# Performance work log

Hardware: AMD Instinct MI355X
Metric: run time of the kernel (lower is better)

The kernel has to match this reference:

```python
import jax, jax.numpy as jnp
import numpy as np

NUM_ELECTIONS = 4096  # number of segments (elections)
N_VOTERS = 1048576
NUM_CANDIDATES = 32
EMB = 128


def setup_inputs() -> dict:
    key = jax.random.key(0)
    ks = jax.random.split(key, 9)
    s = lambda k, sh: jax.random.normal(k, sh, dtype=jnp.float32) * 0.05
    x = jax.random.normal(ks[0], (N_VOTERS, NUM_CANDIDATES), dtype=jnp.float32)
    index = jnp.sort(jax.random.randint(ks[1], (N_VOTERS,), 0, NUM_ELECTIONS)).astype(jnp.int64)
    return {
        "x": x,
        "index": index,
        "lW1": s(ks[2], (NUM_CANDIDATES, EMB)), "lb1": jnp.zeros((EMB,), jnp.float32),
        "lW2": s(ks[3], (EMB, EMB)),            "lb2": jnp.zeros((EMB,), jnp.float32),
        "lW3": s(ks[4], (EMB, EMB)),            "lb3": jnp.zeros((EMB,), jnp.float32),
        "gW1": s(ks[5], (EMB, EMB)),            "gb1": jnp.zeros((EMB,), jnp.float32),
        "gW2": s(ks[6], (EMB, EMB)),            "gb2": jnp.zeros((EMB,), jnp.float32),
        "gW3": s(ks[7], (EMB, NUM_CANDIDATES)), "gb3": jnp.zeros((NUM_CANDIDATES,), jnp.float32),
    }


def reference(x, index, lW1, lb1, lW2, lb2, lW3, lb3, gW1, gb1, gW2, gb2, gW3, gb3):
    # local_nn per voter row: MLP [C, E, E, E], ReLU on hidden layers, plain last
    h = jax.nn.relu(x @ lW1 + lb1)
    h = jax.nn.relu(h @ lW2 + lb2)
    h = h @ lW3 + lb3                      # [N, E]
    # scatter-sum aggregation by election id (DeepSetsAggregation sum reduce)
    agg = jax.ops.segment_sum(h, index, num_segments=NUM_ELECTIONS)  # [S, E]
    # global_nn: MLP [E, E, E, C]
    g = jax.nn.relu(agg @ gW1 + gb1)
    g = jax.nn.relu(g @ gW2 + gb2)
    scores = g @ gW3 + gb3                 # [S, C]
    return jax.nn.log_softmax(scores, axis=-1)
```

## Files before the change

### kernel.cpp

```cpp
#include <hip/hip_runtime.h>
#include <hip/hip_bf16.h>
#include <math.h>

#define N_VOTERS 1048576
#define NUM_CAND 32
#define EMB 128
#define NUM_ELEC 4096

typedef unsigned short u16;
typedef unsigned int u32;
typedef __attribute__((ext_vector_type(8))) short bf16x8;
typedef __attribute__((ext_vector_type(4))) short short4v;
typedef __attribute__((ext_vector_type(4))) float f32x4;

__device__ __forceinline__ u16 f2bf(float f) {
    union { float f; u32 u; } v; v.f = f;
    u32 r = v.u + 0x7FFFu + ((v.u >> 16) & 1u);
    return (u16)(r >> 16);
}
__device__ __forceinline__ u32 pkbf(float f0, float f1) {
    u32 u0 = __float_as_uint(f0) + 0x8000u;
    u32 u1 = __float_as_uint(f1) + 0x8000u;
    return __builtin_amdgcn_perm(u1, u0, 0x07060302u);
}

__global__ void prep_weights(const float* __restrict__ lW1, const float* __restrict__ lW2,
                             const float* __restrict__ lW3,
                             u16* __restrict__ w1t, u16* __restrict__ w2t, u16* __restrict__ w3t) {
    int tid = blockIdx.x * blockDim.x + threadIdx.x;
    if (tid < 4096) {
        int n = tid >> 5, k = tid & 31;
        w1t[tid] = f2bf(lW1[k * EMB + n]);
    }
    {
        int n = tid >> 7, k = tid & 127;
        w2t[tid] = f2bf(lW2[k * EMB + n]);
        w3t[tid] = f2bf(lW3[k * EMB + n]);
    }
}

__global__ __launch_bounds__(256, 4) void local_fused(
    const float* __restrict__ x, const int* __restrict__ idx,
    const float* __restrict__ lb1, const float* __restrict__ lb2, const float* __restrict__ lb3,
    const u16* __restrict__ w1t, const u16* __restrict__ w2t, const u16* __restrict__ w3t,
    float* __restrict__ agg)
{
    constexpr int XSTR = 36;
    constexpr int ASTR = 136;
    __shared__ __align__(16) u16 smem[64 * XSTR + 2 * 64 * ASTR];
    __shared__ int segs[64];
    u16* bufX = smem;
    u16* act1 = smem + 64 * XSTR;
    u16* act2 = act1 + 64 * ASTR;

    const int tid = threadIdx.x;
    const int v0 = blockIdx.x * 64;
    const int lane = tid & 63;
    const int wv = tid >> 6;
    const int qd = lane >> 4;
    const int l15 = lane & 15;
    const int mrow0 = wv * 32 + l15;

    {
        const float4* xin = (const float4*)(x + (size_t)v0 * NUM_CAND);
        #pragma unroll
        for (int i = 0; i < 2; ++i) {
            int F = i * 256 + tid;
            float4 v = xin[F];
            int row = F >> 3, c4 = (F & 7) * 4;
            uint2 pv; pv.x = pkbf(v.x, v.y); pv.y = pkbf(v.z, v.w);
            *(uint2*)(bufX + row * XSTR + c4) = pv;
        }
        if (tid < 64) segs[tid] = idx[v0 + tid];
    }

    bf16x8 wa0 = *(const bf16x8*)(w1t + mrow0 * 32 + qd * 8);
    bf16x8 wa1 = *(const bf16x8*)(w1t + (mrow0 + 16) * 32 + qd * 8);
    f32x4 bA1 = *(const f32x4*)(lb1 + wv * 32 + qd * 4);
    f32x4 bB1 = *(const f32x4*)(lb1 + wv * 32 + 16 + qd * 4);
    __syncthreads();

    #pragma unroll
    for (int nt = 0; nt < 4; ++nt) {
        int vr = nt * 16 + l15;
        union { bf16x8 v; short4v h[2]; } b;
        b.h[0] = *(const short4v*)(bufX + vr * XSTR + qd * 8);
        b.h[1] = *(const short4v*)(bufX + vr * XSTR + qd * 8 + 4);
        f32x4 z = {0.f, 0.f, 0.f, 0.f};
        f32x4 a0 = __builtin_amdgcn_mfma_f32_16x16x32_bf16(wa0, b.v, z, 0, 0, 0);
        f32x4 a1 = __builtin_amdgcn_mfma_f32_16x16x32_bf16(wa1, b.v, z, 0, 0, 0);
        uint2 s0; s0.x = pkbf(fmaxf(a0[0] + bA1[0], 0.f), fmaxf(a0[1] + bA1[1], 0.f));
        s0.y = pkbf(fmaxf(a0[2] + bA1[2], 0.f), fmaxf(a0[3] + bA1[3], 0.f));
        *(uint2*)(act1 + vr * ASTR + wv * 32 + qd * 4) = s0;
        uint2 s1; s1.x = pkbf(fmaxf(a1[0] + bB1[0], 0.f), fmaxf(a1[1] + bB1[1], 0.f));
        s1.y = pkbf(fmaxf(a1[2] + bB1[2], 0.f), fmaxf(a1[3] + bB1[3], 0.f));
        *(uint2*)(act1 + vr * ASTR + wv * 32 + 16 + qd * 4) = s1;
    }

    bf16x8 w2a[2][4];
    #pragma unroll
    for (int t = 0; t < 2; ++t)
        #pragma unroll
        for (int kk = 0; kk < 4; ++kk)
            w2a[t][kk] = *(const bf16x8*)(w2t + (mrow0 + t * 16) * 128 + kk * 32 + qd * 8);
    f32x4 bA2 = *(const f32x4*)(lb2 + wv * 32 + qd * 4);
    f32x4 bB2 = *(const f32x4*)(lb2 + wv * 32 + 16 + qd * 4);
    __syncthreads();

    #pragma unroll
    for (int nt = 0; nt < 4; ++nt) {
        int vr = nt * 16 + l15;
        f32x4 a0 = {0.f, 0.f, 0.f, 0.f}, a1 = {0.f, 0.f, 0.f, 0.f};
        #pragma unroll
        for (int kk = 0; kk < 4; ++kk) {
            bf16x8 b = *(const bf16x8*)(act1 + vr * ASTR + kk * 32 + qd * 8);
            a0 = __builtin_amdgcn_mfma_f32_16x16x32_bf16(w2a[0][kk], b, a0, 0, 0, 0);
            a1 = __builtin_amdgcn_mfma_f32_16x16x32_bf16(w2a[1][kk], b, a1, 0, 0, 0);
        }
        uint2 s0; s0.x = pkbf(fmaxf(a0[0] + bA2[0], 0.f), fmaxf(a0[1] + bA2[1], 0.f));
        s0.y = pkbf(fmaxf(a0[2] + bA2[2], 0.f), fmaxf(a0[3] + bA2[3], 0.f));
        *(uint2*)(act2 + vr * ASTR + wv * 32 + qd * 4) = s0;
        uint2 s1; s1.x = pkbf(fmaxf(a1[0] + bB2[0], 0.f), fmaxf(a1[1] + bB2[1], 0.f));
        s1.y = pkbf(fmaxf(a1[2] + bB2[2], 0.f), fmaxf(a1[3] + bB2[3], 0.f));
        *(uint2*)(act2 + vr * ASTR + wv * 32 + 16 + qd * 4) = s1;
    }

    bf16x8 w3a[2][4];
    #pragma unroll
    for (int t = 0; t < 2; ++t)
        #pragma unroll
        for (int kk = 0; kk < 4; ++kk)
            w3a[t][kk] = *(const bf16x8*)(w3t + (mrow0 + t * 16) * 128 + kk * 32 + qd * 8);
    f32x4 bA3 = *(const f32x4*)(lb3 + wv * 32 + qd * 4);
    f32x4 bB3 = *(const f32x4*)(lb3 + wv * 32 + 16 + qd * 4);
    __syncthreads();

    float fs0[4] = {0.f, 0.f, 0.f, 0.f}, fs1[4] = {0.f, 0.f, 0.f, 0.f};
    int cnt = 0;
    int cur = segs[0];
    float* const aggb = agg + (size_t)wv * 32 + qd * 4;

    auto flush = [&]() {
        float t[8];
        #pragma unroll
        for (int r = 0; r < 4; ++r) { t[r] = fs0[r]; t[4 + r] = fs1[r]; }
        #pragma unroll
        for (int d = 1; d < 16; d <<= 1)
            #pragma unroll
            for (int r = 0; r < 8; ++r) t[r] += __shfl_xor(t[r], d, 16);
        if (l15 == 0) {
            float c = (float)(cnt * 16);
            float* p = aggb + (size_t)cur * EMB;
            #pragma unroll
            for (int r = 0; r < 4; ++r) atomicAdd(p + r,      fmaf(bA3[r], c, t[r]));
            #pragma unroll
            for (int r = 0; r < 4; ++r) atomicAdd(p + 16 + r, fmaf(bB3[r], c, t[4 + r]));
        }
        #pragma unroll
        for (int r = 0; r < 4; ++r) { fs0[r] = 0.f; fs1[r] = 0.f; }
        cnt = 0;
    };

    #pragma unroll
    for (int nt = 0; nt < 4; ++nt) {
        int vr = nt * 16 + l15;
        f32x4 a0 = {0.f, 0.f, 0.f, 0.f}, a1 = {0.f, 0.f, 0.f, 0.f};
        #pragma unroll
        for (int kk = 0; kk < 4; ++kk) {
            bf16x8 b = *(const bf16x8*)(act2 + vr * ASTR + kk * 32 + qd * 8);
            a0 = __builtin_amdgcn_mfma_f32_16x16x32_bf16(w3a[0][kk], b, a0, 0, 0, 0);
            a1 = __builtin_amdgcn_mfma_f32_16x16x32_bf16(w3a[1][kk], b, a1, 0, 0, 0);
        }
        int sg = segs[nt * 16 + l15];
        int first = __builtin_amdgcn_readfirstlane(sg);
        unsigned long long bal = __ballot(sg == first);
        if (bal == ~0ull) {
            if (first != cur) {
                if (cnt > 0) flush();
                cur = first;
            }
            #pragma unroll
            for (int r = 0; r < 4; ++r) { fs0[r] += a0[r]; fs1[r] += a1[r]; }
            ++cnt;
        } else {
            if (cnt > 0) flush();
            float v0a[4], v1a[4];
            #pragma unroll
            for (int r = 0; r < 4; ++r) { v0a[r] = a0[r] + bA3[r]; v1a[r] = a1[r] + bB3[r]; }
            #pragma unroll
            for (int d = 1; d < 16; d <<= 1) {
                int so = __shfl_up(sg, d, 16);
                bool ok = (l15 >= d) && (so == sg);
                #pragma unroll
                for (int r = 0; r < 4; ++r) {
                    float o0 = __shfl_up(v0a[r], d, 16); if (ok) v0a[r] += o0;
                    float o1 = __shfl_up(v1a[r], d, 16); if (ok) v1a[r] += o1;
                }
            }
            int sgn = __shfl_down(sg, 1, 16);
            bool isend = (l15 == 15) || (sgn != sg);
            if (isend) {
                float* p = aggb + (size_t)sg * EMB;
                #pragma unroll
                for (int r = 0; r < 4; ++r) atomicAdd(p + r,      v0a[r]);
                #pragma unroll
                for (int r = 0; r < 4; ++r) atomicAdd(p + 16 + r, v1a[r]);
            }
            cur = __shfl(sg, 15, 16);
        }
    }
    if (cnt > 0) flush();
}

__global__ __launch_bounds__(256) void global_mlp(
    const float* __restrict__ agg,
    const float* __restrict__ gW1, const float* __restrict__ gb1,
    const float* __restrict__ gW2, const float* __restrict__ gb2,
    const float* __restrict__ gW3, const float* __restrict__ gb3,
    float* __restrict__ out)
{
    __shared__ float actA[8 * 128];
    __shared__ float actB[8 * 128];
    __shared__ float sc[8 * 32];
    const int tid = threadIdx.x;
    const int s0 = blockIdx.x * 8;

    #pragma unroll
    for (int i = 0; i < 4; ++i) {
        int f = i * 256 + tid;
        actA[f] = agg[(size_t)s0 * 128 + f];
    }
    __syncthreads();

    const int j = tid & 127, g = tid >> 7;
    {
        float acc[4];
        #pragma unroll
        for (int si = 0; si < 4; ++si) acc[si] = gb1[j];
        #pragma unroll 8
        for (int k = 0; k < 128; ++k) {
            float w = gW1[k * 128 + j];
            #pragma unroll
            for (int si = 0; si < 4; ++si) acc[si] += actA[(g * 4 + si) * 128 + k] * w;
        }
        #pragma unroll
        for (int si = 0; si < 4; ++si) actB[(g * 4 + si) * 128 + j] = fmaxf(acc[si], 0.f);
    }
    __syncthreads();
    {
        float acc[4];
        #pragma unroll
        for (int si = 0; si < 4; ++si) acc[si] = gb2[j];
        #pragma unroll 8
        for (int k = 0; k < 128; ++k) {
            float w = gW2[k * 128 + j];
            #pragma unroll
            for (int si = 0; si < 4; ++si) acc[si] += actB[(g * 4 + si) * 128 + k] * w;
        }
        #pragma unroll
        for (int si = 0; si < 4; ++si) actA[(g * 4 + si) * 128 + j] = fmaxf(acc[si], 0.f);
    }
    __syncthreads();
    {
        int c = tid & 31, sg = tid >> 5;
        float a3 = gb3[c];
        #pragma unroll 8
        for (int k = 0; k < 128; ++k) a3 += actA[sg * 128 + k] * gW3[k * 32 + c];
        sc[sg * 32 + c] = a3;
    }
    __syncthreads();
    {
        int c = tid & 31, sg = tid >> 5;
        float v = sc[sg * 32 + c];
        float m = v;
        #pragma unroll
        for (int off = 16; off >= 1; off >>= 1) m = fmaxf(m, __shfl_xor(m, off, 32));
        float e = expf(v - m);
        float sum = e;
        #pragma unroll
        for (int off = 16; off >= 1; off >>= 1) sum += __shfl_xor(sum, off, 32);
        out[(size_t)(s0 + sg) * 32 + c] = (v - m) - logf(sum);
    }
}

extern "C" void kernel_launch(void* const* d_in, const int* in_sizes, int n_in,
                              void* d_out, int out_size, void* d_ws, size_t ws_size,
                              hipStream_t stream) {
    const float* x   = (const float*)d_in[0];
    const int*   idx = (const int*)d_in[1];
    const float* lW1 = (const float*)d_in[2];
    const float* lb1 = (const float*)d_in[3];
    const float* lW2 = (const float*)d_in[4];
    const float* lb2 = (const float*)d_in[5];
    const float* lW3 = (const float*)d_in[6];
    const float* lb3 = (const float*)d_in[7];
    const float* gW1 = (const float*)d_in[8];
    const float* gb1 = (const float*)d_in[9];
    const float* gW2 = (const float*)d_in[10];
    const float* gb2 = (const float*)d_in[11];
    const float* gW3 = (const float*)d_in[12];
    const float* gb3 = (const float*)d_in[13];
    float* out = (float*)d_out;

    float* agg = (float*)d_ws;
    u16* w1t = (u16*)((char*)d_ws + (size_t)NUM_ELEC * EMB * 4);
    u16* w2t = w1t + 128 * 32;
    u16* w3t = w2t + 128 * 128;

    hipMemsetAsync(d_ws, 0, (size_t)NUM_ELEC * EMB * sizeof(float), stream);
    prep_weights<<<64, 256, 0, stream>>>(lW1, lW2, lW3, w1t, w2t, w3t);
    local_fused<<<N_VOTERS / 64, 256, 0, stream>>>(x, idx, lb1, lb2, lb3, w1t, w2t, w3t, agg);
    global_mlp<<<NUM_ELEC / 8, 256, 0, stream>>>(agg, gW1, gb1, gW2, gb2, gW3, gb3, out);
}
```

Baseline: 352.2 us.

## Keep local MLP activations in registers with per-wave full-width tiles and LDS-resident weights

Restructures the local MLP kernel so each wave computes all 128 output features for its own 64 voters. Inter-layer activations are passed through cross-lane shuffles instead of LDS round trips, and all three weight matrices sit in shared memory for 512-thread blocks. The last-layer bias is folded into the global MLP through per-segment voter counts, and the next x tile is prefetched into registers. It removes the LDS activation staging and block-wide barriers between layers, at the cost of many shuffles, high register pressure from the 8x4 accumulators, and reloading the weights into LDS for every block.

```diff
diff --git a/kernel.cpp b/kernel.cpp
--- a/kernel.cpp
+++ b/kernel.cpp
@@ -10,8 +10,9 @@
 typedef unsigned short u16;
 typedef unsigned int u32;
 typedef __attribute__((ext_vector_type(8))) short bf16x8;
-typedef __attribute__((ext_vector_type(4))) short short4v;
 typedef __attribute__((ext_vector_type(4))) float f32x4;
+
+union U4 { u32 u[4]; bf16x8 v; };
 
 __device__ __forceinline__ u16 f2bf(float f) {
     union { float f; u32 u; } v; v.f = f;
@@ -39,181 +40,246 @@
     }
 }
 
-__global__ __launch_bounds__(256, 4) void local_fused(
+__global__ __launch_bounds__(512, 4) void local_fused(
     const float* __restrict__ x, const int* __restrict__ idx,
-    const float* __restrict__ lb1, const float* __restrict__ lb2, const float* __restrict__ lb3,
+    const float* __restrict__ lb1, const float* __restrict__ lb2,
     const u16* __restrict__ w1t, const u16* __restrict__ w2t, const u16* __restrict__ w3t,
-    float* __restrict__ agg)
+    float* __restrict__ agg, float* __restrict__ cntf)
 {
-    constexpr int XSTR = 36;
-    constexpr int ASTR = 136;
-    __shared__ __align__(16) u16 smem[64 * XSTR + 2 * 64 * ASTR];
-    __shared__ int segs[64];
-    u16* bufX = smem;
-    u16* act1 = smem + 64 * XSTR;
-    u16* act2 = act1 + 64 * ASTR;
+    __shared__ __align__(16) u16 w1s[128 * 32];
+    __shared__ __align__(16) u16 w2s[128 * 128];
+    __shared__ __align__(16) u16 w3s[128 * 128];
+    __shared__ __align__(16) float lb1s[128], lb2s[128];
 
     const int tid = threadIdx.x;
-    const int v0 = blockIdx.x * 64;
+
+    {
+        const uint4* s2 = (const uint4*)w2t; uint4* d2 = (uint4*)w2s;
+        const uint4* s3 = (const uint4*)w3t; uint4* d3 = (uint4*)w3s;
+        #pragma unroll
+        for (int i = 0; i < 4; ++i) {
+            d2[tid + i * 512] = s2[tid + i * 512];
+            d3[tid + i * 512] = s3[tid + i * 512];
+        }
+        ((uint4*)w1s)[tid] = ((const uint4*)w1t)[tid];
+        if (tid < 128) { lb1s[tid] = lb1[tid]; lb2s[tid] = lb2[tid]; }
+    }
+    __syncthreads();
+
     const int lane = tid & 63;
     const int wv = tid >> 6;
     const int qd = lane >> 4;
     const int l15 = lane & 15;
-    const int mrow0 = wv * 32 + l15;
-
-    {
-        const float4* xin = (const float4*)(x + (size_t)v0 * NUM_CAND);
-        #pragma unroll
-        for (int i = 0; i < 2; ++i) {
-            int F = i * 256 + tid;
-            float4 v = xin[F];
-            int row = F >> 3, c4 = (F & 7) * 4;
-            uint2 pv; pv.x = pkbf(v.x, v.y); pv.y = pkbf(v.z, v.w);
-            *(uint2*)(bufX + row * XSTR + c4) = pv;
-        }
-        if (tid < 64) segs[tid] = idx[v0 + tid];
-    }
-
-    bf16x8 wa0 = *(const bf16x8*)(w1t + mrow0 * 32 + qd * 8);
-    bf16x8 wa1 = *(const bf16x8*)(w1t + (mrow0 + 16) * 32 + qd * 8);
-    f32x4 bA1 = *(const f32x4*)(lb1 + wv * 32 + qd * 4);
-    f32x4 bB1 = *(const f32x4*)(lb1 + wv * 32 + 16 + qd * 4);
-    __syncthreads();
-
+    const int vb = blockIdx.x * 512 + wv * 64;
+
+    const int s0l = ((qd & 1) << 5) + l15;
+    const int s1l = s0l + 16;
+    const bool hi = (qd >> 1) != 0;
+
+    float fs[8][4];
     #pragma unroll
+    for (int m = 0; m < 8; ++m)
+        #pragma unroll
+        for (int r = 0; r < 4; ++r) fs[m][r] = 0.f;
+    float cntv = 0.f;
+    int cur = idx[vb];
+
+    const float* xr0 = x + (size_t)(vb + l15) * NUM_CAND + qd * 8;
+    float4 xa = *(const float4*)xr0;
+    float4 xb = *(const float4*)(xr0 + 4);
+
+    #pragma unroll 1
     for (int nt = 0; nt < 4; ++nt) {
-        int vr = nt * 16 + l15;
-        union { bf16x8 v; short4v h[2]; } b;
-        b.h[0] = *(const short4v*)(bufX + vr * XSTR + qd * 8);
-        b.h[1] = *(const short4v*)(bufX + vr * XSTR + qd * 8 + 4);
-        f32x4 z = {0.f, 0.f, 0.f, 0.f};
-        f32x4 a0 = __builtin_amdgcn_mfma_f32_16x16x32_bf16(wa0, b.v, z, 0, 0, 0);
-        f32x4 a1 = __builtin_amdgcn_mfma_f32_16x16x32_bf16(wa1, b.v, z, 0, 0, 0);
-        uint2 s0; s0.x = pkbf(fmaxf(a0[0] + bA1[0], 0.f), fmaxf(a0[1] + bA1[1], 0.f));
-        s0.y = pkbf(fmaxf(a0[2] + bA1[2], 0.f), fmaxf(a0[3] + bA1[3], 0.f));
-        *(uint2*)(act1 + vr * ASTR + wv * 32 + qd * 4) = s0;
-        uint2 s1; s1.x = pkbf(fmaxf(a1[0] + bB1[0], 0.f), fmaxf(a1[1] + bB1[1], 0.f));
-        s1.y = pkbf(fmaxf(a1[2] + bB1[2], 0.f), fmaxf(a1[3] + bB1[3], 0.f));
-        *(uint2*)(act1 + vr * ASTR + wv * 32 + 16 + qd * 4) = s1;
-    }
-
-    bf16x8 w2a[2][4];
-    #pragma unroll
-    for (int t = 0; t < 2; ++t)
-        #pragma unroll
-        for (int kk = 0; kk < 4; ++kk)
-            w2a[t][kk] = *(const bf16x8*)(w2t + (mrow0 + t * 16) * 128 + kk * 32 + qd * 8);
-    f32x4 bA2 = *(const f32x4*)(lb2 + wv * 32 + qd * 4);
-    f32x4 bB2 = *(const f32x4*)(lb2 + wv * 32 + 16 + qd * 4);
-    __syncthreads();
-
-    #pragma unroll
-    for (int nt = 0; nt < 4; ++nt) {
-        int vr = nt * 16 + l15;
-        f32x4 a0 = {0.f, 0.f, 0.f, 0.f}, a1 = {0.f, 0.f, 0.f, 0.f};
+        int sg = idx[vb + nt * 16 + l15];
+        int ntn = (nt < 3) ? nt + 1 : 3;
+        const float* xrn = x + (size_t)(vb + ntn * 16 + l15) * NUM_CAND + qd * 8;
+        float4 xa_n = *(const float4*)xrn;
+        float4 xb_n = *(const float4*)(xrn + 4);
+
+        U4 B1; B1.u[0] = pkbf(xa.x, xa.y); B1.u[1] = pkbf(xa.z, xa.w);
+        B1.u[2] = pkbf(xb.x, xb.y); B1.u[3] = pkbf(xb.z, xb.w);
+
+        f32x4 D[8];
+        #pragma unroll
+        for (int mt = 0; mt < 8; ++mt) {
+            bf16x8 A = *(const bf16x8*)(w1s + (mt * 16 + l15) * 32 + qd * 8);
+            f32x4 z = {0.f, 0.f, 0.f, 0.f};
+            D[mt] = __builtin_amdgcn_mfma_f32_16x16x32_bf16(A, B1.v, z, 0, 0, 0);
+        }
+        u32 P[8][2];
+        #pragma unroll
+        for (int mt = 0; mt < 8; ++mt) {
+            f32x4 b = *(const f32x4*)(lb1s + mt * 16 + qd * 4);
+            float v0 = fmaxf(D[mt][0] + b[0], 0.f), v1 = fmaxf(D[mt][1] + b[1], 0.f);
+            float v2 = fmaxf(D[mt][2] + b[2], 0.f), v3 = fmaxf(D[mt][3] + b[3], 0.f);
+            P[mt][0] = pkbf(v0, v1); P[mt][1] = pkbf(v2, v3);
+        }
+        U4 Bf[4];
         #pragma unroll
         for (int kk = 0; kk < 4; ++kk) {
-            bf16x8 b = *(const bf16x8*)(act1 + vr * ASTR + kk * 32 + qd * 8);
-            a0 = __builtin_amdgcn_mfma_f32_16x16x32_bf16(w2a[0][kk], b, a0, 0, 0, 0);
-            a1 = __builtin_amdgcn_mfma_f32_16x16x32_bf16(w2a[1][kk], b, a1, 0, 0, 0);
-        }
-        uint2 s0; s0.x = pkbf(fmaxf(a0[0] + bA2[0], 0.f), fmaxf(a0[1] + bA2[1], 0.f));
-        s0.y = pkbf(fmaxf(a0[2] + bA2[2], 0.f), fmaxf(a0[3] + bA2[3], 0.f));
-        *(uint2*)(act2 + vr * ASTR + wv * 32 + qd * 4) = s0;
-        uint2 s1; s1.x = pkbf(fmaxf(a1[0] + bB2[0], 0.f), fmaxf(a1[1] + bB2[1], 0.f));
-        s1.y = pkbf(fmaxf(a1[2] + bB2[2], 0.f), fmaxf(a1[3] + bB2[3], 0.f));
-        *(uint2*)(act2 + vr * ASTR + wv * 32 + 16 + qd * 4) = s1;
-    }
-
-    bf16x8 w3a[2][4];
-    #pragma unroll
-    for (int t = 0; t < 2; ++t)
-        #pragma unroll
-        for (int kk = 0; kk < 4; ++kk)
-            w3a[t][kk] = *(const bf16x8*)(w3t + (mrow0 + t * 16) * 128 + kk * 32 + qd * 8);
-    f32x4 bA3 = *(const f32x4*)(lb3 + wv * 32 + qd * 4);
-    f32x4 bB3 = *(const f32x4*)(lb3 + wv * 32 + 16 + qd * 4);
-    __syncthreads();
-
-    float fs0[4] = {0.f, 0.f, 0.f, 0.f}, fs1[4] = {0.f, 0.f, 0.f, 0.f};
-    int cnt = 0;
-    int cur = segs[0];
-    float* const aggb = agg + (size_t)wv * 32 + qd * 4;
-
-    auto flush = [&]() {
-        float t[8];
-        #pragma unroll
-        for (int r = 0; r < 4; ++r) { t[r] = fs0[r]; t[4 + r] = fs1[r]; }
-        #pragma unroll
-        for (int d = 1; d < 16; d <<= 1)
-            #pragma unroll
-            for (int r = 0; r < 8; ++r) t[r] += __shfl_xor(t[r], d, 16);
-        if (l15 == 0) {
-            float c = (float)(cnt * 16);
-            float* p = aggb + (size_t)cur * EMB;
-            #pragma unroll
-            for (int r = 0; r < 4; ++r) atomicAdd(p + r,      fmaf(bA3[r], c, t[r]));
-            #pragma unroll
-            for (int r = 0; r < 4; ++r) atomicAdd(p + 16 + r, fmaf(bB3[r], c, t[4 + r]));
-        }
-        #pragma unroll
-        for (int r = 0; r < 4; ++r) { fs0[r] = 0.f; fs1[r] = 0.f; }
-        cnt = 0;
-    };
-
-    #pragma unroll
-    for (int nt = 0; nt < 4; ++nt) {
-        int vr = nt * 16 + l15;
-        f32x4 a0 = {0.f, 0.f, 0.f, 0.f}, a1 = {0.f, 0.f, 0.f, 0.f};
+            u32 e0 = __shfl(P[2 * kk][0], s0l, 64), o0 = __shfl(P[2 * kk + 1][0], s0l, 64);
+            u32 e1 = __shfl(P[2 * kk][1], s0l, 64), o1 = __shfl(P[2 * kk + 1][1], s0l, 64);
+            u32 e2 = __shfl(P[2 * kk][0], s1l, 64), o2 = __shfl(P[2 * kk + 1][0], s1l, 64);
+            u32 e3 = __shfl(P[2 * kk][1], s1l, 64), o3 = __shfl(P[2 * kk + 1][1], s1l, 64);
+            Bf[kk].u[0] = hi ? o0 : e0; Bf[kk].u[1] = hi ? o1 : e1;
+            Bf[kk].u[2] = hi ? o2 : e2; Bf[kk].u[3] = hi ? o3 : e3;
+        }
+        #pragma unroll
+        for (int mt = 0; mt < 8; ++mt) {
+            f32x4 a = {0.f, 0.f, 0.f, 0.f};
+            #pragma unroll
+            for (int kk = 0; kk < 4; ++kk) {
+                bf16x8 A = *(const bf16x8*)(w2s + (mt * 16 + l15) * 128 + kk * 32 + qd * 8);
+                a = __builtin_amdgcn_mfma_f32_16x16x32_bf16(A, Bf[kk].v, a, 0, 0, 0);
+            }
+            D[mt] = a;
+        }
+        #pragma unroll
+        for (int mt = 0; mt < 8; ++mt) {
+            f32x4 b = *(const f32x4*)(lb2s + mt * 16 + qd * 4);
+            float v0 = fmaxf(D[mt][0] + b[0], 0.f), v1 = fmaxf(D[mt][1] + b[1], 0.f);
+            float v2 = fmaxf(D[mt][2] + b[2], 0.f), v3 = fmaxf(D[mt][3] + b[3], 0.f);
+            P[mt][0] = pkbf(v0, v1); P[mt][1] = pkbf(v2, v3);
+        }
         #pragma unroll
         for (int kk = 0; kk < 4; ++kk) {
-            bf16x8 b = *(const bf16x8*)(act2 + vr * ASTR + kk * 32 + qd * 8);
-            a0 = __builtin_amdgcn_mfma_f32_16x16x32_bf16(w3a[0][kk], b, a0, 0, 0, 0);
-            a1 = __builtin_amdgcn_mfma_f32_16x16x32_bf16(w3a[1][kk], b, a1, 0, 0, 0);
-        }
-        int sg = segs[nt * 16 + l15];
+            u32 e0 = __shfl(P[2 * kk][0], s0l, 64), o0 = __shfl(P[2 * kk + 1][0], s0l, 64);
+            u32 e1 = __shfl(P[2 * kk][1], s0l, 64), o1 = __shfl(P[2 * kk + 1][1], s0l, 64);
+            u32 e2 = __shfl(P[2 * kk][0], s1l, 64), o2 = __shfl(P[2 * kk + 1][0], s1l, 64);
+            u32 e3 = __shfl(P[2 * kk][1], s1l, 64), o3 = __shfl(P[2 * kk + 1][1], s1l, 64);
+            Bf[kk].u[0] = hi ? o0 : e0; Bf[kk].u[1] = hi ? o1 : e1;
+            Bf[kk].u[2] = hi ? o2 : e2; Bf[kk].u[3] = hi ? o3 : e3;
+        }
+        #pragma unroll
+        for (int mt = 0; mt < 8; ++mt) {
+            f32x4 a = {0.f, 0.f, 0.f, 0.f};
+            #pragma unroll
+            for (int kk = 0; kk < 4; ++kk) {
+                bf16x8 A = *(const bf16x8*)(w3s + (mt * 16 + l15) * 128 + kk * 32 + qd * 8);
+                a = __builtin_amdgcn_mfma_f32_16x16x32_bf16(A, Bf[kk].v, a, 0, 0, 0);
+            }
+            D[mt] = a;
+        }
+
+        xa = xa_n; xb = xb_n;
+
         int first = __builtin_amdgcn_readfirstlane(sg);
         unsigned long long bal = __ballot(sg == first);
         if (bal == ~0ull) {
             if (first != cur) {
-                if (cnt > 0) flush();
+                if (cntv > 0.f) {
+                    float t[8][4];
+                    #pragma unroll
+                    for (int m = 0; m < 8; ++m)
+                        #pragma unroll
+                        for (int r = 0; r < 4; ++r) t[m][r] = fs[m][r];
+                    #pragma unroll
+                    for (int d = 1; d < 16; d <<= 1)
+                        #pragma unroll
+                        for (int m = 0; m < 8; ++m)
+                            #pragma unroll
+                            for (int r = 0; r < 4; ++r) t[m][r] += __shfl_xor(t[m][r], d, 16);
+                    if (l15 == 0) {
+                        float* p = agg + (size_t)cur * EMB + qd * 4;
+                        #pragma unroll
+                        for (int m = 0; m < 8; ++m)
+                            #pragma unroll
+                            for (int r = 0; r < 4; ++r) atomicAdd(p + m * 16 + r, t[m][r]);
+                        if (qd == 0) atomicAdd(cntf + cur, cntv);
+                    }
+                    #pragma unroll
+                    for (int m = 0; m < 8; ++m)
+                        #pragma unroll
+                        for (int r = 0; r < 4; ++r) fs[m][r] = 0.f;
+                    cntv = 0.f;
+                }
                 cur = first;
             }
             #pragma unroll
-            for (int r = 0; r < 4; ++r) { fs0[r] += a0[r]; fs1[r] += a1[r]; }
-            ++cnt;
+            for (int m = 0; m < 8; ++m)
+                #pragma unroll
+                for (int r = 0; r < 4; ++r) fs[m][r] += D[m][r];
+            cntv += 16.f;
         } else {
-            if (cnt > 0) flush();
-            float v0a[4], v1a[4];
-            #pragma unroll
-            for (int r = 0; r < 4; ++r) { v0a[r] = a0[r] + bA3[r]; v1a[r] = a1[r] + bB3[r]; }
+            if (cntv > 0.f) {
+                float t[8][4];
+                #pragma unroll
+                for (int m = 0; m < 8; ++m)
+                    #pragma unroll
+                    for (int r = 0; r < 4; ++r) t[m][r] = fs[m][r];
+                #pragma unroll
+                for (int d = 1; d < 16; d <<= 1)
+                    #pragma unroll
+                    for (int m = 0; m < 8; ++m)
+                        #pragma unroll
+                        for (int r = 0; r < 4; ++r) t[m][r] += __shfl_xor(t[m][r], d, 16);
+                if (l15 == 0) {
+                    float* p = agg + (size_t)cur * EMB + qd * 4;
+                    #pragma unroll
+                    for (int m = 0; m < 8; ++m)
+                        #pragma unroll
+                        for (int r = 0; r < 4; ++r) atomicAdd(p + m * 16 + r, t[m][r]);
+                    if (qd == 0) atomicAdd(cntf + cur, cntv);
+                }
+                #pragma unroll
+                for (int m = 0; m < 8; ++m)
+                    #pragma unroll
+                    for (int r = 0; r < 4; ++r) fs[m][r] = 0.f;
+                cntv = 0.f;
+            }
+            float one = 1.f;
             #pragma unroll
             for (int d = 1; d < 16; d <<= 1) {
                 int so = __shfl_up(sg, d, 16);
                 bool ok = (l15 >= d) && (so == sg);
                 #pragma unroll
-                for (int r = 0; r < 4; ++r) {
-                    float o0 = __shfl_up(v0a[r], d, 16); if (ok) v0a[r] += o0;
-                    float o1 = __shfl_up(v1a[r], d, 16); if (ok) v1a[r] += o1;
-                }
+                for (int m = 0; m < 8; ++m)
+                    #pragma unroll
+                    for (int r = 0; r < 4; ++r) {
+                        float o = __shfl_up(D[m][r], d, 16);
+                        if (ok) D[m][r] += o;
+                    }
+                float oc = __shfl_up(one, d, 16);
+                if (ok) one += oc;
             }
             int sgn = __shfl_down(sg, 1, 16);
             bool isend = (l15 == 15) || (sgn != sg);
             if (isend) {
-                float* p = aggb + (size_t)sg * EMB;
-                #pragma unroll
-                for (int r = 0; r < 4; ++r) atomicAdd(p + r,      v0a[r]);
-                #pragma unroll
-                for (int r = 0; r < 4; ++r) atomicAdd(p + 16 + r, v1a[r]);
+                float* p = agg + (size_t)sg * EMB + qd * 4;
+                #pragma unroll
+                for (int m = 0; m < 8; ++m)
+                    #pragma unroll
+                    for (int r = 0; r < 4; ++r) atomicAdd(p + m * 16 + r, D[m][r]);
+                if (qd == 0) atomicAdd(cntf + sg, one);
             }
             cur = __shfl(sg, 15, 16);
         }
     }
-    if (cnt > 0) flush();
+    if (cntv > 0.f) {
+        float t[8][4];
+        #pragma unroll
+        for (int m = 0; m < 8; ++m)
+            #pragma unroll
+            for (int r = 0; r < 4; ++r) t[m][r] = fs[m][r];
+        #pragma unroll
+        for (int d = 1; d < 16; d <<= 1)
+            #pragma unroll
+            for (int m = 0; m < 8; ++m)
+                #pragma unroll
+                for (int r = 0; r < 4; ++r) t[m][r] += __shfl_xor(t[m][r], d, 16);
+        if (l15 == 0) {
+            float* p = agg + (size_t)cur * EMB + qd * 4;
+            #pragma unroll
+            for (int m = 0; m < 8; ++m)
+                #pragma unroll
+                for (int r = 0; r < 4; ++r) atomicAdd(p + m * 16 + r, t[m][r]);
+            if (qd == 0) atomicAdd(cntf + cur, cntv);
+        }
+    }
 }
 
 __global__ __launch_bounds__(256) void global_mlp(
-    const float* __restrict__ agg,
+    const float* __restrict__ agg, const float* __restrict__ cntf, const float* __restrict__ lb3,
     const float* __restrict__ gW1, const float* __restrict__ gb1,
     const float* __restrict__ gW2, const float* __restrict__ gb2,
     const float* __restrict__ gW3, const float* __restrict__ gb3,
@@ -228,7 +294,7 @@
     #pragma unroll
     for (int i = 0; i < 4; ++i) {
         int f = i * 256 + tid;
-        actA[f] = agg[(size_t)s0 * 128 + f];
+        actA[f] = agg[(size_t)s0 * 128 + f] + cntf[s0 + (f >> 7)] * lb3[f & 127];
     }
     __syncthreads();
 
@@ -302,13 +368,14 @@
     const float* gb3 = (const float*)d_in[13];
     float* out = (float*)d_out;
 
-    float* agg = (float*)d_ws;
-    u16* w1t = (u16*)((char*)d_ws + (size_t)NUM_ELEC * EMB * 4);
+    float* agg  = (float*)d_ws;
+    float* cntf = agg + (size_t)NUM_ELEC * EMB;
+    u16* w1t = (u16*)(cntf + NUM_ELEC);
     u16* w2t = w1t + 128 * 32;
     u16* w3t = w2t + 128 * 128;
 
-    hipMemsetAsync(d_ws, 0, (size_t)NUM_ELEC * EMB * sizeof(float), stream);
+    hipMemsetAsync(d_ws, 0, ((size_t)NUM_ELEC * EMB + NUM_ELEC) * sizeof(float), stream);
     prep_weights<<<64, 256, 0, stream>>>(lW1, lW2, lW3, w1t, w2t, w3t);
-    local_fused<<<N_VOTERS / 64, 256, 0, stream>>>(x, idx, lb1, lb2, lb3, w1t, w2t, w3t, agg);
-    global_mlp<<<NUM_ELEC / 8, 256, 0, stream>>>(agg, gW1, gb1, gW2, gb2, gW3, gb3, out);
-}
+    local_fused<<<N_VOTERS / 512, 512, 0, stream>>>(x, idx, lb1, lb2, w1t, w2t, w3t, agg, cntf);
+    global_mlp<<<NUM_ELEC / 8, 256, 0, stream>>>(agg, cntf, lb3, gW1, gb1, gW2, gb2, gW3, gb3, out);
+}
```

After: 762.6 us. 2.17x slower.

## Make local MLP blocks persistent over 512 voters with register-resident weights

Applied to the files above, without the earlier changes.

The local MLP kernel now uses 128-thread blocks that each process 512 voters in eight groups of 64. Each wave holds a 64-column slice of all three weight matrices in registers, loaded once per block instead of once per 64 voters. The next x tile is prefetched straight into registers, which drops the x staging buffer in shared memory. Biases are folded into the MFMA accumulator, and the third layer accumulates directly into running MFMA accumulators for uniform segments. The lb3 bias term moves to the global kernel through a per-segment count array. In exchange, register pressure rises sharply and the grid has far fewer blocks, which may reduce occupancy and latency hiding.

```diff
diff --git a/kernel.cpp b/kernel.cpp
--- a/kernel.cpp
+++ b/kernel.cpp
@@ -10,7 +10,6 @@
 typedef unsigned short u16;
 typedef unsigned int u32;
 typedef __attribute__((ext_vector_type(8))) short bf16x8;
-typedef __attribute__((ext_vector_type(4))) short short4v;
 typedef __attribute__((ext_vector_type(4))) float f32x4;
 
 __device__ __forceinline__ u16 f2bf(float f) {
@@ -39,181 +38,182 @@
     }
 }
 
-__global__ __launch_bounds__(256, 4) void local_fused(
+__global__ __launch_bounds__(128, 2) void local_fused(
     const float* __restrict__ x, const int* __restrict__ idx,
-    const float* __restrict__ lb1, const float* __restrict__ lb2, const float* __restrict__ lb3,
+    const float* __restrict__ lb1, const float* __restrict__ lb2,
     const u16* __restrict__ w1t, const u16* __restrict__ w2t, const u16* __restrict__ w3t,
-    float* __restrict__ agg)
+    float* __restrict__ agg, float* __restrict__ cntf)
 {
-    constexpr int XSTR = 36;
     constexpr int ASTR = 136;
-    __shared__ __align__(16) u16 smem[64 * XSTR + 2 * 64 * ASTR];
-    __shared__ int segs[64];
-    u16* bufX = smem;
-    u16* act1 = smem + 64 * XSTR;
-    u16* act2 = act1 + 64 * ASTR;
+    __shared__ __align__(16) u16 act1[64 * ASTR];
+    __shared__ __align__(16) u16 act2[64 * ASTR];
 
     const int tid = threadIdx.x;
-    const int v0 = blockIdx.x * 64;
     const int lane = tid & 63;
     const int wv = tid >> 6;
     const int qd = lane >> 4;
     const int l15 = lane & 15;
-    const int mrow0 = wv * 32 + l15;
-
-    {
-        const float4* xin = (const float4*)(x + (size_t)v0 * NUM_CAND);
-        #pragma unroll
-        for (int i = 0; i < 2; ++i) {
-            int F = i * 256 + tid;
-            float4 v = xin[F];
-            int row = F >> 3, c4 = (F & 7) * 4;
-            uint2 pv; pv.x = pkbf(v.x, v.y); pv.y = pkbf(v.z, v.w);
-            *(uint2*)(bufX + row * XSTR + c4) = pv;
-        }
-        if (tid < 64) segs[tid] = idx[v0 + tid];
-    }
-
-    bf16x8 wa0 = *(const bf16x8*)(w1t + mrow0 * 32 + qd * 8);
-    bf16x8 wa1 = *(const bf16x8*)(w1t + (mrow0 + 16) * 32 + qd * 8);
-    f32x4 bA1 = *(const f32x4*)(lb1 + wv * 32 + qd * 4);
-    f32x4 bB1 = *(const f32x4*)(lb1 + wv * 32 + 16 + qd * 4);
-    __syncthreads();
-
+    const int h64 = wv * 64;
+
+    bf16x8 w1a[4], w2a[4][4], w3a[4][4];
+    f32x4 b1f[4], b2f[4];
     #pragma unroll
-    for (int nt = 0; nt < 4; ++nt) {
-        int vr = nt * 16 + l15;
-        union { bf16x8 v; short4v h[2]; } b;
-        b.h[0] = *(const short4v*)(bufX + vr * XSTR + qd * 8);
-        b.h[1] = *(const short4v*)(bufX + vr * XSTR + qd * 8 + 4);
-        f32x4 z = {0.f, 0.f, 0.f, 0.f};
-        f32x4 a0 = __builtin_amdgcn_mfma_f32_16x16x32_bf16(wa0, b.v, z, 0, 0, 0);
-        f32x4 a1 = __builtin_amdgcn_mfma_f32_16x16x32_bf16(wa1, b.v, z, 0, 0, 0);
-        uint2 s0; s0.x = pkbf(fmaxf(a0[0] + bA1[0], 0.f), fmaxf(a0[1] + bA1[1], 0.f));
-        s0.y = pkbf(fmaxf(a0[2] + bA1[2], 0.f), fmaxf(a0[3] + bA1[3], 0.f));
-        *(uint2*)(act1 + vr * ASTR + wv * 32 + qd * 4) = s0;
-        uint2 s1; s1.x = pkbf(fmaxf(a1[0] + bB1[0], 0.f), fmaxf(a1[1] + bB1[1], 0.f));
-        s1.y = pkbf(fmaxf(a1[2] + bB1[2], 0.f), fmaxf(a1[3] + bB1[3], 0.f));
-        *(uint2*)(act1 + vr * ASTR + wv * 32 + 16 + qd * 4) = s1;
-    }
-
-    bf16x8 w2a[2][4];
+    for (int mt = 0; mt < 4; ++mt) {
+        int mrow = h64 + mt * 16 + l15;
+        w1a[mt] = *(const bf16x8*)(w1t + mrow * 32 + qd * 8);
+        #pragma unroll
+        for (int kk = 0; kk < 4; ++kk) {
+            w2a[mt][kk] = *(const bf16x8*)(w2t + mrow * 128 + kk * 32 + qd * 8);
+            w3a[mt][kk] = *(const bf16x8*)(w3t + mrow * 128 + kk * 32 + qd * 8);
+        }
+        b1f[mt] = *(const f32x4*)(lb1 + h64 + mt * 16 + qd * 4);
+        b2f[mt] = *(const f32x4*)(lb2 + h64 + mt * 16 + qd * 4);
+    }
+
+    const int vblk = blockIdx.x * 512;
+    f32x4 accR[4];
     #pragma unroll
-    for (int t = 0; t < 2; ++t)
-        #pragma unroll
-        for (int kk = 0; kk < 4; ++kk)
-            w2a[t][kk] = *(const bf16x8*)(w2t + (mrow0 + t * 16) * 128 + kk * 32 + qd * 8);
-    f32x4 bA2 = *(const f32x4*)(lb2 + wv * 32 + qd * 4);
-    f32x4 bB2 = *(const f32x4*)(lb2 + wv * 32 + 16 + qd * 4);
-    __syncthreads();
-
-    #pragma unroll
-    for (int nt = 0; nt < 4; ++nt) {
-        int vr = nt * 16 + l15;
-        f32x4 a0 = {0.f, 0.f, 0.f, 0.f}, a1 = {0.f, 0.f, 0.f, 0.f};
-        #pragma unroll
-        for (int kk = 0; kk < 4; ++kk) {
-            bf16x8 b = *(const bf16x8*)(act1 + vr * ASTR + kk * 32 + qd * 8);
-            a0 = __builtin_amdgcn_mfma_f32_16x16x32_bf16(w2a[0][kk], b, a0, 0, 0, 0);
-            a1 = __builtin_amdgcn_mfma_f32_16x16x32_bf16(w2a[1][kk], b, a1, 0, 0, 0);
-        }
-        uint2 s0; s0.x = pkbf(fmaxf(a0[0] + bA2[0], 0.f), fmaxf(a0[1] + bA2[1], 0.f));
-        s0.y = pkbf(fmaxf(a0[2] + bA2[2], 0.f), fmaxf(a0[3] + bA2[3], 0.f));
-        *(uint2*)(act2 + vr * ASTR + wv * 32 + qd * 4) = s0;
-        uint2 s1; s1.x = pkbf(fmaxf(a1[0] + bB2[0], 0.f), fmaxf(a1[1] + bB2[1], 0.f));
-        s1.y = pkbf(fmaxf(a1[2] + bB2[2], 0.f), fmaxf(a1[3] + bB2[3], 0.f));
-        *(uint2*)(act2 + vr * ASTR + wv * 32 + 16 + qd * 4) = s1;
-    }
-
-    bf16x8 w3a[2][4];
-    #pragma unroll
-    for (int t = 0; t < 2; ++t)
-        #pragma unroll
-        for (int kk = 0; kk < 4; ++kk)
-            w3a[t][kk] = *(const bf16x8*)(w3t + (mrow0 + t * 16) * 128 + kk * 32 + qd * 8);
-    f32x4 bA3 = *(const f32x4*)(lb3 + wv * 32 + qd * 4);
-    f32x4 bB3 = *(const f32x4*)(lb3 + wv * 32 + 16 + qd * 4);
-    __syncthreads();
-
-    float fs0[4] = {0.f, 0.f, 0.f, 0.f}, fs1[4] = {0.f, 0.f, 0.f, 0.f};
-    int cnt = 0;
-    int cur = segs[0];
-    float* const aggb = agg + (size_t)wv * 32 + qd * 4;
+    for (int mt = 0; mt < 4; ++mt) accR[mt] = (f32x4){0.f, 0.f, 0.f, 0.f};
+    float cntv = 0.f;
+    int cur = idx[vblk];
 
     auto flush = [&]() {
-        float t[8];
-        #pragma unroll
-        for (int r = 0; r < 4; ++r) { t[r] = fs0[r]; t[4 + r] = fs1[r]; }
         #pragma unroll
         for (int d = 1; d < 16; d <<= 1)
             #pragma unroll
-            for (int r = 0; r < 8; ++r) t[r] += __shfl_xor(t[r], d, 16);
+            for (int mt = 0; mt < 4; ++mt)
+                #pragma unroll
+                for (int r = 0; r < 4; ++r) accR[mt][r] += __shfl_xor(accR[mt][r], d, 16);
         if (l15 == 0) {
-            float c = (float)(cnt * 16);
-            float* p = aggb + (size_t)cur * EMB;
-            #pragma unroll
-            for (int r = 0; r < 4; ++r) atomicAdd(p + r,      fmaf(bA3[r], c, t[r]));
-            #pragma unroll
-            for (int r = 0; r < 4; ++r) atomicAdd(p + 16 + r, fmaf(bB3[r], c, t[4 + r]));
-        }
-        #pragma unroll
-        for (int r = 0; r < 4; ++r) { fs0[r] = 0.f; fs1[r] = 0.f; }
-        cnt = 0;
+            float* p = agg + (size_t)cur * EMB + h64 + qd * 4;
+            #pragma unroll
+            for (int mt = 0; mt < 4; ++mt)
+                #pragma unroll
+                for (int r = 0; r < 4; ++r) atomicAdd(p + mt * 16 + r, accR[mt][r]);
+            if (wv == 0 && qd == 0) atomicAdd(cntf + cur, cntv);
+        }
+        #pragma unroll
+        for (int mt = 0; mt < 4; ++mt) accR[mt] = (f32x4){0.f, 0.f, 0.f, 0.f};
+        cntv = 0.f;
     };
 
-    #pragma unroll
-    for (int nt = 0; nt < 4; ++nt) {
-        int vr = nt * 16 + l15;
-        f32x4 a0 = {0.f, 0.f, 0.f, 0.f}, a1 = {0.f, 0.f, 0.f, 0.f};
-        #pragma unroll
-        for (int kk = 0; kk < 4; ++kk) {
-            bf16x8 b = *(const bf16x8*)(act2 + vr * ASTR + kk * 32 + qd * 8);
-            a0 = __builtin_amdgcn_mfma_f32_16x16x32_bf16(w3a[0][kk], b, a0, 0, 0, 0);
-            a1 = __builtin_amdgcn_mfma_f32_16x16x32_bf16(w3a[1][kk], b, a1, 0, 0, 0);
-        }
-        int sg = segs[nt * 16 + l15];
-        int first = __builtin_amdgcn_readfirstlane(sg);
-        unsigned long long bal = __ballot(sg == first);
-        if (bal == ~0ull) {
-            if (first != cur) {
-                if (cnt > 0) flush();
-                cur = first;
+    const float* xp0 = x + (size_t)(vblk + l15) * NUM_CAND + qd * 8;
+    float4 xa = *(const float4*)xp0;
+    float4 xb = *(const float4*)(xp0 + 4);
+
+    #pragma unroll 1
+    for (int g = 0; g < 8; ++g) {
+        const int vg = vblk + g * 64;
+        #pragma unroll
+        for (int nt = 0; nt < 4; ++nt) {
+            int tnext = g * 4 + nt + 1; if (tnext > 31) tnext = 31;
+            const float* xn = x + (size_t)(vblk + tnext * 16 + l15) * NUM_CAND + qd * 8;
+            float4 xa_n = *(const float4*)xn;
+            float4 xb_n = *(const float4*)(xn + 4);
+
+            union { u32 u[4]; bf16x8 v; } B1;
+            B1.u[0] = pkbf(xa.x, xa.y); B1.u[1] = pkbf(xa.z, xa.w);
+            B1.u[2] = pkbf(xb.x, xb.y); B1.u[3] = pkbf(xb.z, xb.w);
+            u16* wr = act1 + (nt * 16 + l15) * ASTR + h64 + qd * 4;
+            #pragma unroll
+            for (int mt = 0; mt < 4; ++mt) {
+                f32x4 a = __builtin_amdgcn_mfma_f32_16x16x32_bf16(w1a[mt], B1.v, b1f[mt], 0, 0, 0);
+                uint2 s;
+                s.x = pkbf(fmaxf(a[0], 0.f), fmaxf(a[1], 0.f));
+                s.y = pkbf(fmaxf(a[2], 0.f), fmaxf(a[3], 0.f));
+                *(uint2*)(wr + mt * 16) = s;
             }
-            #pragma unroll
-            for (int r = 0; r < 4; ++r) { fs0[r] += a0[r]; fs1[r] += a1[r]; }
-            ++cnt;
-        } else {
-            if (cnt > 0) flush();
-            float v0a[4], v1a[4];
-            #pragma unroll
-            for (int r = 0; r < 4; ++r) { v0a[r] = a0[r] + bA3[r]; v1a[r] = a1[r] + bB3[r]; }
-            #pragma unroll
-            for (int d = 1; d < 16; d <<= 1) {
-                int so = __shfl_up(sg, d, 16);
-                bool ok = (l15 >= d) && (so == sg);
-                #pragma unroll
-                for (int r = 0; r < 4; ++r) {
-                    float o0 = __shfl_up(v0a[r], d, 16); if (ok) v0a[r] += o0;
-                    float o1 = __shfl_up(v1a[r], d, 16); if (ok) v1a[r] += o1;
-                }
+            xa = xa_n; xb = xb_n;
+        }
+        __syncthreads();
+        #pragma unroll
+        for (int nt = 0; nt < 4; ++nt) {
+            const u16* rd = act1 + (nt * 16 + l15) * ASTR + qd * 8;
+            bf16x8 B2[4];
+            #pragma unroll
+            for (int kk = 0; kk < 4; ++kk) B2[kk] = *(const bf16x8*)(rd + kk * 32);
+            u16* wr = act2 + (nt * 16 + l15) * ASTR + h64 + qd * 4;
+            #pragma unroll
+            for (int mt = 0; mt < 4; ++mt) {
+                f32x4 a = b2f[mt];
+                #pragma unroll
+                for (int kk = 0; kk < 4; ++kk)
+                    a = __builtin_amdgcn_mfma_f32_16x16x32_bf16(w2a[mt][kk], B2[kk], a, 0, 0, 0);
+                uint2 s;
+                s.x = pkbf(fmaxf(a[0], 0.f), fmaxf(a[1], 0.f));
+                s.y = pkbf(fmaxf(a[2], 0.f), fmaxf(a[3], 0.f));
+                *(uint2*)(wr + mt * 16) = s;
             }
-            int sgn = __shfl_down(sg, 1, 16);
-            bool isend = (l15 == 15) || (sgn != sg);
-            if (isend) {
-                float* p = aggb + (size_t)sg * EMB;
-                #pragma unroll
-                for (int r = 0; r < 4; ++r) atomicAdd(p + r,      v0a[r]);
-                #pragma unroll
-                for (int r = 0; r < 4; ++r) atomicAdd(p + 16 + r, v1a[r]);
+        }
+        __syncthreads();
+        #pragma unroll 1
+        for (int nt = 0; nt < 4; ++nt) {
+            int sg = idx[vg + nt * 16 + l15];
+            const u16* rd = act2 + (nt * 16 + l15) * ASTR + qd * 8;
+            bf16x8 B3[4];
+            #pragma unroll
+            for (int kk = 0; kk < 4; ++kk) B3[kk] = *(const bf16x8*)(rd + kk * 32);
+            int first = __builtin_amdgcn_readfirstlane(sg);
+            bool uni = (__ballot(sg == first) == ~0ull);
+            if (uni) {
+                if (first != cur) {
+                    if (cntv > 0.f) flush();
+                    cur = first;
+                }
+                #pragma unroll
+                for (int mt = 0; mt < 4; ++mt) {
+                    f32x4 a = accR[mt];
+                    #pragma unroll
+                    for (int kk = 0; kk < 4; ++kk)
+                        a = __builtin_amdgcn_mfma_f32_16x16x32_bf16(w3a[mt][kk], B3[kk], a, 0, 0, 0);
+                    accR[mt] = a;
+                }
+                cntv += 16.f;
+            } else {
+                if (cntv > 0.f) flush();
+                f32x4 D[4];
+                #pragma unroll
+                for (int mt = 0; mt < 4; ++mt) {
+                    f32x4 a = {0.f, 0.f, 0.f, 0.f};
+                    #pragma unroll
+                    for (int kk = 0; kk < 4; ++kk)
+                        a = __builtin_amdgcn_mfma_f32_16x16x32_bf16(w3a[mt][kk], B3[kk], a, 0, 0, 0);
+                    D[mt] = a;
+                }
+                float one = 1.f;
+                #pragma unroll
+                for (int d = 1; d < 16; d <<= 1) {
+                    int so = __shfl_up(sg, d, 16);
+                    bool ok = (l15 >= d) && (so == sg);
+                    #pragma unroll
+                    for (int mt = 0; mt < 4; ++mt)
+                        #pragma unroll
+                        for (int r = 0; r < 4; ++r) {
+                            float o = __shfl_up(D[mt][r], d, 16);
+                            if (ok) D[mt][r] += o;
+                        }
+                    float oc = __shfl_up(one, d, 16);
+                    if (ok) one += oc;
+                }
+                int sgn = __shfl_down(sg, 1, 16);
+                bool isend = (l15 == 15) || (sgn != sg);
+                if (isend) {
+                    float* p = agg + (size_t)sg * EMB + h64 + qd * 4;
+                    #pragma unroll
+                    for (int mt = 0; mt < 4; ++mt)
+                        #pragma unroll
+                        for (int r = 0; r < 4; ++r) atomicAdd(p + mt * 16 + r, D[mt][r]);
+                    if (wv == 0 && qd == 0) atomicAdd(cntf + sg, one);
+                }
+                cur = __shfl(sg, 15, 16);
             }
-            cur = __shfl(sg, 15, 16);
-        }
-    }
-    if (cnt > 0) flush();
+        }
+    }
+    if (cntv > 0.f) flush();
 }
 
 __global__ __launch_bounds__(256) void global_mlp(
-    const float* __restrict__ agg,
+    const float* __restrict__ agg, const float* __restrict__ cntf, const float* __restrict__ lb3,
     const float* __restrict__ gW1, const float* __restrict__ gb1,
     const float* __restrict__ gW2, const float* __restrict__ gb2,
     const float* __restrict__ gW3, const float* __restrict__ gb3,
@@ -228,7 +228,7 @@
     #pragma unroll
     for (int i = 0; i < 4; ++i) {
         int f = i * 256 + tid;
-        actA[f] = agg[(size_t)s0 * 128 + f];
+        actA[f] = agg[(size_t)s0 * 128 + f] + cntf[s0 + (f >> 7)] * lb3[f & 127];
     }
     __syncthreads();
 
@@ -302,13 +302,14 @@
     const float* gb3 = (const float*)d_in[13];
     float* out = (float*)d_out;
 
-    float* agg = (float*)d_ws;
-    u16* w1t = (u16*)((char*)d_ws + (size_t)NUM_ELEC * EMB * 4);
+    float* agg  = (float*)d_ws;
+    float* cntf = agg + (size_t)NUM_ELEC * EMB;
+    u16* w1t = (u16*)(cntf + NUM_ELEC);
     u16* w2t = w1t + 128 * 32;
     u16* w3t = w2t + 128 * 128;
 
-    hipMemsetAsync(d_ws, 0, (size_t)NUM_ELEC * EMB * sizeof(float), stream);
+    hipMemsetAsync(d_ws, 0, ((size_t)NUM_ELEC * EMB + NUM_ELEC) * sizeof(float), stream);
     prep_weights<<<64, 256, 0, stream>>>(lW1, lW2, lW3, w1t, w2t, w3t);
-    local_fused<<<N_VOTERS / 64, 256, 0, stream>>>(x, idx, lb1, lb2, lb3, w1t, w2t, w3t, agg);
-    global_mlp<<<NUM_ELEC / 8, 256, 0, stream>>>(agg, gW1, gb1, gW2, gb2, gW3, gb3, out);
-}
+    local_fused<<<N_VOTERS / 512, 128, 0, stream>>>(x, idx, lb1, lb2, w1t, w2t, w3t, agg, cntf);
+    global_mlp<<<NUM_ELEC / 8, 256, 0, stream>>>(agg, cntf, lb3, gW1, gb1, gW2, gb2, gW3, gb3, out);
+}
```

Measured after the change: 396.2 us. 12.5% more time.
